# Kernel optimization log

Hardware: AMD Instinct MI355X
Metric: run time of the kernel (lower is better)

## Reference

```python
import jax, jax.numpy as jnp
import numpy as np

RADIUS = 2
ITERATION = 8
KSIZE = 2 * RADIUS + 1


def _side_window_kernels():
    """Build the 8 directional box kernels exactly as in the torch module.
    Returns (8, 1, k, k) float32: order L, R, U, D, NW, NE, SW, SE."""
    r, k = RADIUS, KSIZE
    ones = np.ones((k, k), np.float32)
    L = ones.copy(); L[:, r + 1:] = 0
    R = ones.copy(); R[:, :r] = 0
    U = ones.copy(); U[r + 1:, :] = 0
    D = ones.copy(); D[:r, :] = 0
    # diagonal kernels are cloned from U/D BEFORE normalization (as in source)
    NW, NE, SW, SE = U.copy(), U.copy(), D.copy(), D.copy()
    n_half = (r + 1) * k
    L, R, U, D = L / n_half, R / n_half, U / n_half, D / n_half
    NW[:, r + 1:] = 0; NE[:, :r] = 0; SW[:, r + 1:] = 0; SE[:, :r] = 0
    n_quad = float((r + 1) ** 2)
    NW, NE, SW, SE = NW / n_quad, NE / n_quad, SW / n_quad, SE / n_quad
    return np.stack([L, R, U, D, NW, NE, SW, SE])[:, None]  # (8,1,k,k)


def setup_inputs() -> dict:
    key = jax.random.key(0)
    # HWC image with pixel values in [0, 255)
    img = jax.random.uniform(key, (2048, 2048, 3), dtype=jnp.float32) * 255.0
    return {"img": img}


def reference(img) -> jnp.ndarray:
    kern = jnp.asarray(_side_window_kernels())          # (8,1,k,k)
    x0 = jnp.transpose(img, (2, 0, 1))[:, None]          # (C,1,H,W): channels as batch

    def step(im, _):
        # replicate padding, then valid conv with all 8 directional kernels at once
        p = jnp.pad(im, ((0, 0), (0, 0), (RADIUS, RADIUS), (RADIUS, RADIUS)), mode="edge")
        conv = jax.lax.conv_general_dilated(p, kern, (1, 1), "VALID")  # (C,8,H,W)
        d = conv - im                                    # broadcast (C,1,H,W)->(C,8,H,W)
        idx = jnp.argmin(jnp.abs(d), axis=1, keepdims=True)
        dm = jnp.take_along_axis(d, idx, axis=1)         # (C,1,H,W)
        return im + dm, None

    res, _ = jax.lax.scan(step, x0, None, length=ITERATION)
    diff = jnp.abs(x0 - res)[:, 0]                       # (C,H,W)
    out = jnp.transpose(diff, (1, 2, 0))                 # (H,W,C)
    return jnp.clip(out, 0.0, 255.0)
```

## Files before the change

kernel.cpp:

```cpp
#include <hip/hip_runtime.h>


static constexpr int H  = 2048;
static constexpr int W  = 2048;
static constexpr int C  = 3;
static constexpr int WC = W * C;

template<bool FINAL>
__global__ __launch_bounds__(256)
void swf_step4(const float* __restrict__ src, float* __restrict__ dst,
               const float* __restrict__ x0) {
  const int col4 = (blockIdx.x * 256 + threadIdx.x) * 4;
  const int h    = blockIdx.y;

  const float w15 = 1.0f / 15.0f;
  const float w9  = 1.0f / 9.0f;

  float acc[4][8];
#pragma unroll
  for (int k = 0; k < 4; ++k)
#pragma unroll
    for (int m = 0; m < 8; ++m) acc[k][m] = 0.0f;
  float center[4];

  const bool fastc = (col4 >= 8) && (col4 <= WC - 12);
  if (fastc) {
#pragma unroll
    for (int i = 0; i < 5; ++i) {
      int hy = h + i - 2;
      hy = hy < 0 ? 0 : (hy > H - 1 ? H - 1 : hy);
      const float4* rp = (const float4*)(src + (size_t)hy * WC + (col4 - 8));
      const float4 q0 = rp[0], q1 = rp[1], q2 = rp[2], q3 = rp[3], q4 = rp[4];
      const float r[20] = {q0.x,q0.y,q0.z,q0.w, q1.x,q1.y,q1.z,q1.w,
                           q2.x,q2.y,q2.z,q2.w, q3.x,q3.y,q3.z,q3.w,
                           q4.x,q4.y,q4.z,q4.w};
#pragma unroll
      for (int k = 0; k < 4; ++k) {
        const float t0 = r[k+2], t1 = r[k+5], t2 = r[k+8],
                    t3 = r[k+11], t4 = r[k+14];
        float* a = acc[k];
        if (i == 2) center[k] = t2;
        a[0]=__builtin_fmaf(w15,t0,a[0]); a[0]=__builtin_fmaf(w15,t1,a[0]); a[0]=__builtin_fmaf(w15,t2,a[0]);
        a[1]=__builtin_fmaf(w15,t2,a[1]); a[1]=__builtin_fmaf(w15,t3,a[1]); a[1]=__builtin_fmaf(w15,t4,a[1]);
        if (i <= 2) {
          a[2]=__builtin_fmaf(w15,t0,a[2]); a[2]=__builtin_fmaf(w15,t1,a[2]); a[2]=__builtin_fmaf(w15,t2,a[2]);
          a[2]=__builtin_fmaf(w15,t3,a[2]); a[2]=__builtin_fmaf(w15,t4,a[2]);
          a[4]=__builtin_fmaf(w9,t0,a[4]); a[4]=__builtin_fmaf(w9,t1,a[4]); a[4]=__builtin_fmaf(w9,t2,a[4]);
          a[5]=__builtin_fmaf(w9,t2,a[5]); a[5]=__builtin_fmaf(w9,t3,a[5]); a[5]=__builtin_fmaf(w9,t4,a[5]);
        }
        if (i >= 2) {
          a[3]=__builtin_fmaf(w15,t0,a[3]); a[3]=__builtin_fmaf(w15,t1,a[3]); a[3]=__builtin_fmaf(w15,t2,a[3]);
          a[3]=__builtin_fmaf(w15,t3,a[3]); a[3]=__builtin_fmaf(w15,t4,a[3]);
          a[6]=__builtin_fmaf(w9,t0,a[6]); a[6]=__builtin_fmaf(w9,t1,a[6]); a[6]=__builtin_fmaf(w9,t2,a[6]);
          a[7]=__builtin_fmaf(w9,t2,a[7]); a[7]=__builtin_fmaf(w9,t3,a[7]); a[7]=__builtin_fmaf(w9,t4,a[7]);
        }
      }
    }
  } else {
#pragma unroll
    for (int k = 0; k < 4; ++k) {
      const int col = col4 + k;
      const int w   = col / 3;
      const int c   = col - w * 3;
      int cj[5];
#pragma unroll
      for (int j = 0; j < 5; ++j) {
        int wj = w + j - 2;
        wj = wj < 0 ? 0 : (wj > W - 1 ? W - 1 : wj);
        cj[j] = wj * 3 + c;
      }
      float* a = acc[k];
#pragma unroll
      for (int i = 0; i < 5; ++i) {
        int hy = h + i - 2;
        hy = hy < 0 ? 0 : (hy > H - 1 ? H - 1 : hy);
        const float* r = src + (size_t)hy * WC;
        const float t0 = r[cj[0]], t1 = r[cj[1]], t2 = r[cj[2]],
                    t3 = r[cj[3]], t4 = r[cj[4]];
        if (i == 2) center[k] = t2;
        a[0]=__builtin_fmaf(w15,t0,a[0]); a[0]=__builtin_fmaf(w15,t1,a[0]); a[0]=__builtin_fmaf(w15,t2,a[0]);
        a[1]=__builtin_fmaf(w15,t2,a[1]); a[1]=__builtin_fmaf(w15,t3,a[1]); a[1]=__builtin_fmaf(w15,t4,a[1]);
        if (i <= 2) {
          a[2]=__builtin_fmaf(w15,t0,a[2]); a[2]=__builtin_fmaf(w15,t1,a[2]); a[2]=__builtin_fmaf(w15,t2,a[2]);
          a[2]=__builtin_fmaf(w15,t3,a[2]); a[2]=__builtin_fmaf(w15,t4,a[2]);
          a[4]=__builtin_fmaf(w9,t0,a[4]); a[4]=__builtin_fmaf(w9,t1,a[4]); a[4]=__builtin_fmaf(w9,t2,a[4]);
          a[5]=__builtin_fmaf(w9,t2,a[5]); a[5]=__builtin_fmaf(w9,t3,a[5]); a[5]=__builtin_fmaf(w9,t4,a[5]);
        }
        if (i >= 2) {
          a[3]=__builtin_fmaf(w15,t0,a[3]); a[3]=__builtin_fmaf(w15,t1,a[3]); a[3]=__builtin_fmaf(w15,t2,a[3]);
          a[3]=__builtin_fmaf(w15,t3,a[3]); a[3]=__builtin_fmaf(w15,t4,a[3]);
          a[6]=__builtin_fmaf(w9,t0,a[6]); a[6]=__builtin_fmaf(w9,t1,a[6]); a[6]=__builtin_fmaf(w9,t2,a[6]);
          a[7]=__builtin_fmaf(w9,t2,a[7]); a[7]=__builtin_fmaf(w9,t3,a[7]); a[7]=__builtin_fmaf(w9,t4,a[7]);
        }
      }
    }
  }

  float o[4];
#pragma unroll
  for (int k = 0; k < 4; ++k) {
    float best  = acc[k][0] - center[k];
    float besta = fabsf(best);
#pragma unroll
    for (int m = 1; m < 8; ++m) {
      const float d = acc[k][m] - center[k];
      const float a = fabsf(d);
      if (a < besta) { besta = a; best = d; }
    }
    const float res = center[k] + best;
    if (FINAL) {
      const float xv = x0[(size_t)h * WC + col4 + k];
      float diff = fabsf(xv - res);
      o[k] = diff > 255.0f ? 255.0f : diff;
    } else {
      o[k] = res;
    }
  }
  float4 ov;
  ov.x = o[0]; ov.y = o[1]; ov.z = o[2]; ov.w = o[3];
  *(float4*)(dst + (size_t)h * WC + col4) = ov;
}

extern "C" void kernel_launch(void* const* d_in, const int* in_sizes, int n_in,
                              void* d_out, int out_size, void* d_ws, size_t ws_size,
                              hipStream_t stream) {
  const float* x0  = (const float*)d_in[0];
  float*       out = (float*)d_out;
  float*       ws  = (float*)d_ws;

  dim3 grid(WC / 1024, H);
  dim3 block(256);

  swf_step4<false><<<grid, block, 0, stream>>>(x0,  ws,  nullptr);
  swf_step4<false><<<grid, block, 0, stream>>>(ws,  out, nullptr);
  swf_step4<false><<<grid, block, 0, stream>>>(out, ws,  nullptr);
  swf_step4<false><<<grid, block, 0, stream>>>(ws,  out, nullptr);
  swf_step4<false><<<grid, block, 0, stream>>>(out, ws,  nullptr);
  swf_step4<false><<<grid, block, 0, stream>>>(ws,  out, nullptr);
  swf_step4<false><<<grid, block, 0, stream>>>(out, ws,  nullptr);
  swf_step4<true ><<<grid, block, 0, stream>>>(ws,  out, x0);
}
```

Measured before the change: 463.6 us.

## Process eight rows per thread with rolling register window of input rows

Each thread now computes eight consecutive output rows, keeping a rolling 5-row window of float4 loads in registers so each input row is loaded once per thread instead of five times. The grid shrinks in the row dimension by the same factor. This cuts redundant global/L2 load traffic and instruction issue for loads, at the cost of higher register pressure (25 float4 plus accumulators) and fewer blocks for latency hiding.

New measurement: 509.2 us. 1.1x slower.

```diff
diff --git a/kernel.cpp b/kernel.cpp
--- a/kernel.cpp
+++ b/kernel.cpp
@@ -1,124 +1,186 @@
 #include <hip/hip_runtime.h>
 
 
-static constexpr int H  = 2048;
-static constexpr int W  = 2048;
-static constexpr int C  = 3;
-static constexpr int WC = W * C;
+static constexpr int H   = 2048;
+static constexpr int W   = 2048;
+static constexpr int C   = 3;
+static constexpr int WC  = W * C;
+static constexpr int RPT = 8;
 
 template<bool FINAL>
 __global__ __launch_bounds__(256)
-void swf_step4(const float* __restrict__ src, float* __restrict__ dst,
-               const float* __restrict__ x0) {
+void swf_roll(const float* __restrict__ src, float* __restrict__ dst,
+              const float* __restrict__ x0) {
   const int col4 = (blockIdx.x * 256 + threadIdx.x) * 4;
-  const int h    = blockIdx.y;
+  const int h0   = blockIdx.y * RPT;
 
   const float w15 = 1.0f / 15.0f;
   const float w9  = 1.0f / 9.0f;
 
-  float acc[4][8];
-#pragma unroll
-  for (int k = 0; k < 4; ++k)
-#pragma unroll
-    for (int m = 0; m < 8; ++m) acc[k][m] = 0.0f;
-  float center[4];
-
   const bool fastc = (col4 >= 8) && (col4 <= WC - 12);
   if (fastc) {
-#pragma unroll
-    for (int i = 0; i < 5; ++i) {
-      int hy = h + i - 2;
-      hy = hy < 0 ? 0 : (hy > H - 1 ? H - 1 : hy);
-      const float4* rp = (const float4*)(src + (size_t)hy * WC + (col4 - 8));
-      const float4 q0 = rp[0], q1 = rp[1], q2 = rp[2], q3 = rp[3], q4 = rp[4];
-      const float r[20] = {q0.x,q0.y,q0.z,q0.w, q1.x,q1.y,q1.z,q1.w,
-                           q2.x,q2.y,q2.z,q2.w, q3.x,q3.y,q3.z,q3.w,
-                           q4.x,q4.y,q4.z,q4.w};
+    const float* colbase = src + (col4 - 8);
+    float4 q[5][5];
+
+#pragma unroll
+    for (int p = 0; p < 4; ++p) {
+      int hy = h0 + p - 2;
+      hy = hy < 0 ? 0 : hy;
+      const float4* rp = (const float4*)(colbase + (size_t)hy * WC);
+#pragma unroll
+      for (int j = 0; j < 5; ++j) q[p][j] = rp[j];
+    }
+
+#pragma unroll
+    for (int t = 0; t < RPT; ++t) {
+      {
+        int hy = h0 + t + 2;
+        hy = hy > H - 1 ? H - 1 : hy;
+        const float4* rp = (const float4*)(colbase + (size_t)hy * WC);
+#pragma unroll
+        for (int j = 0; j < 5; ++j) q[(t + 4) % 5][j] = rp[j];
+      }
+
+      float acc[4][8];
+#pragma unroll
+      for (int k = 0; k < 4; ++k)
+#pragma unroll
+        for (int m = 0; m < 8; ++m) acc[k][m] = 0.0f;
+      float center[4];
+
+#pragma unroll
+      for (int i = 0; i < 5; ++i) {
+        const int s = (t + i) % 5;
+        const float r[20] = {q[s][0].x,q[s][0].y,q[s][0].z,q[s][0].w,
+                             q[s][1].x,q[s][1].y,q[s][1].z,q[s][1].w,
+                             q[s][2].x,q[s][2].y,q[s][2].z,q[s][2].w,
+                             q[s][3].x,q[s][3].y,q[s][3].z,q[s][3].w,
+                             q[s][4].x,q[s][4].y,q[s][4].z,q[s][4].w};
+#pragma unroll
+        for (int k = 0; k < 4; ++k) {
+          const float t0 = r[k+2], t1 = r[k+5], t2 = r[k+8],
+                      t3 = r[k+11], t4 = r[k+14];
+          float* a = acc[k];
+          if (i == 2) center[k] = t2;
+          a[0]=__builtin_fmaf(w15,t0,a[0]); a[0]=__builtin_fmaf(w15,t1,a[0]); a[0]=__builtin_fmaf(w15,t2,a[0]);
+          a[1]=__builtin_fmaf(w15,t2,a[1]); a[1]=__builtin_fmaf(w15,t3,a[1]); a[1]=__builtin_fmaf(w15,t4,a[1]);
+          if (i <= 2) {
+            a[2]=__builtin_fmaf(w15,t0,a[2]); a[2]=__builtin_fmaf(w15,t1,a[2]); a[2]=__builtin_fmaf(w15,t2,a[2]);
+            a[2]=__builtin_fmaf(w15,t3,a[2]); a[2]=__builtin_fmaf(w15,t4,a[2]);
+            a[4]=__builtin_fmaf(w9,t0,a[4]); a[4]=__builtin_fmaf(w9,t1,a[4]); a[4]=__builtin_fmaf(w9,t2,a[4]);
+            a[5]=__builtin_fmaf(w9,t2,a[5]); a[5]=__builtin_fmaf(w9,t3,a[5]); a[5]=__builtin_fmaf(w9,t4,a[5]);
+          }
+          if (i >= 2) {
+            a[3]=__builtin_fmaf(w15,t0,a[3]); a[3]=__builtin_fmaf(w15,t1,a[3]); a[3]=__builtin_fmaf(w15,t2,a[3]);
+            a[3]=__builtin_fmaf(w15,t3,a[3]); a[3]=__builtin_fmaf(w15,t4,a[3]);
+            a[6]=__builtin_fmaf(w9,t0,a[6]); a[6]=__builtin_fmaf(w9,t1,a[6]); a[6]=__builtin_fmaf(w9,t2,a[6]);
+            a[7]=__builtin_fmaf(w9,t2,a[7]); a[7]=__builtin_fmaf(w9,t3,a[7]); a[7]=__builtin_fmaf(w9,t4,a[7]);
+          }
+        }
+      }
+
+      const int y = h0 + t;
+      float4 xv4;
+      if (FINAL) xv4 = *(const float4*)(x0 + (size_t)y * WC + col4);
+      float o[4];
 #pragma unroll
       for (int k = 0; k < 4; ++k) {
-        const float t0 = r[k+2], t1 = r[k+5], t2 = r[k+8],
-                    t3 = r[k+11], t4 = r[k+14];
-        float* a = acc[k];
-        if (i == 2) center[k] = t2;
-        a[0]=__builtin_fmaf(w15,t0,a[0]); a[0]=__builtin_fmaf(w15,t1,a[0]); a[0]=__builtin_fmaf(w15,t2,a[0]);
-        a[1]=__builtin_fmaf(w15,t2,a[1]); a[1]=__builtin_fmaf(w15,t3,a[1]); a[1]=__builtin_fmaf(w15,t4,a[1]);
-        if (i <= 2) {
-          a[2]=__builtin_fmaf(w15,t0,a[2]); a[2]=__builtin_fmaf(w15,t1,a[2]); a[2]=__builtin_fmaf(w15,t2,a[2]);
-          a[2]=__builtin_fmaf(w15,t3,a[2]); a[2]=__builtin_fmaf(w15,t4,a[2]);
-          a[4]=__builtin_fmaf(w9,t0,a[4]); a[4]=__builtin_fmaf(w9,t1,a[4]); a[4]=__builtin_fmaf(w9,t2,a[4]);
-          a[5]=__builtin_fmaf(w9,t2,a[5]); a[5]=__builtin_fmaf(w9,t3,a[5]); a[5]=__builtin_fmaf(w9,t4,a[5]);
-        }
-        if (i >= 2) {
-          a[3]=__builtin_fmaf(w15,t0,a[3]); a[3]=__builtin_fmaf(w15,t1,a[3]); a[3]=__builtin_fmaf(w15,t2,a[3]);
-          a[3]=__builtin_fmaf(w15,t3,a[3]); a[3]=__builtin_fmaf(w15,t4,a[3]);
-          a[6]=__builtin_fmaf(w9,t0,a[6]); a[6]=__builtin_fmaf(w9,t1,a[6]); a[6]=__builtin_fmaf(w9,t2,a[6]);
-          a[7]=__builtin_fmaf(w9,t2,a[7]); a[7]=__builtin_fmaf(w9,t3,a[7]); a[7]=__builtin_fmaf(w9,t4,a[7]);
-        }
-      }
+        float best  = acc[k][0] - center[k];
+        float besta = fabsf(best);
+#pragma unroll
+        for (int m = 1; m < 8; ++m) {
+          const float d = acc[k][m] - center[k];
+          const float a = fabsf(d);
+          if (a < besta) { besta = a; best = d; }
+        }
+        const float res = center[k] + best;
+        if (FINAL) {
+          const float xv = (k == 0) ? xv4.x : (k == 1) ? xv4.y
+                         : (k == 2) ? xv4.z : xv4.w;
+          float diff = fabsf(xv - res);
+          o[k] = diff > 255.0f ? 255.0f : diff;
+        } else {
+          o[k] = res;
+        }
+      }
+      float4 ov;
+      ov.x = o[0]; ov.y = o[1]; ov.z = o[2]; ov.w = o[3];
+      *(float4*)(dst + (size_t)y * WC + col4) = ov;
     }
   } else {
+    int cjk[4][5];
 #pragma unroll
     for (int k = 0; k < 4; ++k) {
       const int col = col4 + k;
       const int w   = col / 3;
       const int c   = col - w * 3;
-      int cj[5];
 #pragma unroll
       for (int j = 0; j < 5; ++j) {
         int wj = w + j - 2;
         wj = wj < 0 ? 0 : (wj > W - 1 ? W - 1 : wj);
-        cj[j] = wj * 3 + c;
-      }
-      float* a = acc[k];
-#pragma unroll
-      for (int i = 0; i < 5; ++i) {
-        int hy = h + i - 2;
-        hy = hy < 0 ? 0 : (hy > H - 1 ? H - 1 : hy);
-        const float* r = src + (size_t)hy * WC;
-        const float t0 = r[cj[0]], t1 = r[cj[1]], t2 = r[cj[2]],
-                    t3 = r[cj[3]], t4 = r[cj[4]];
-        if (i == 2) center[k] = t2;
-        a[0]=__builtin_fmaf(w15,t0,a[0]); a[0]=__builtin_fmaf(w15,t1,a[0]); a[0]=__builtin_fmaf(w15,t2,a[0]);
-        a[1]=__builtin_fmaf(w15,t2,a[1]); a[1]=__builtin_fmaf(w15,t3,a[1]); a[1]=__builtin_fmaf(w15,t4,a[1]);
-        if (i <= 2) {
-          a[2]=__builtin_fmaf(w15,t0,a[2]); a[2]=__builtin_fmaf(w15,t1,a[2]); a[2]=__builtin_fmaf(w15,t2,a[2]);
-          a[2]=__builtin_fmaf(w15,t3,a[2]); a[2]=__builtin_fmaf(w15,t4,a[2]);
-          a[4]=__builtin_fmaf(w9,t0,a[4]); a[4]=__builtin_fmaf(w9,t1,a[4]); a[4]=__builtin_fmaf(w9,t2,a[4]);
-          a[5]=__builtin_fmaf(w9,t2,a[5]); a[5]=__builtin_fmaf(w9,t3,a[5]); a[5]=__builtin_fmaf(w9,t4,a[5]);
-        }
-        if (i >= 2) {
-          a[3]=__builtin_fmaf(w15,t0,a[3]); a[3]=__builtin_fmaf(w15,t1,a[3]); a[3]=__builtin_fmaf(w15,t2,a[3]);
-          a[3]=__builtin_fmaf(w15,t3,a[3]); a[3]=__builtin_fmaf(w15,t4,a[3]);
-          a[6]=__builtin_fmaf(w9,t0,a[6]); a[6]=__builtin_fmaf(w9,t1,a[6]); a[6]=__builtin_fmaf(w9,t2,a[6]);
-          a[7]=__builtin_fmaf(w9,t2,a[7]); a[7]=__builtin_fmaf(w9,t3,a[7]); a[7]=__builtin_fmaf(w9,t4,a[7]);
-        }
-      }
+        cjk[k][j] = wj * 3 + c;
+      }
+    }
+    for (int t = 0; t < RPT; ++t) {
+      const int y = h0 + t;
+      float acc[4][8];
+#pragma unroll
+      for (int k = 0; k < 4; ++k)
+#pragma unroll
+        for (int m = 0; m < 8; ++m) acc[k][m] = 0.0f;
+      float center[4];
+#pragma unroll
+      for (int k = 0; k < 4; ++k) {
+        float* a = acc[k];
+#pragma unroll
+        for (int i = 0; i < 5; ++i) {
+          int hy = y + i - 2;
+          hy = hy < 0 ? 0 : (hy > H - 1 ? H - 1 : hy);
+          const float* r = src + (size_t)hy * WC;
+          const float t0 = r[cjk[k][0]], t1 = r[cjk[k][1]], t2 = r[cjk[k][2]],
+                      t3 = r[cjk[k][3]], t4 = r[cjk[k][4]];
+          if (i == 2) center[k] = t2;
+          a[0]=__builtin_fmaf(w15,t0,a[0]); a[0]=__builtin_fmaf(w15,t1,a[0]); a[0]=__builtin_fmaf(w15,t2,a[0]);
+          a[1]=__builtin_fmaf(w15,t2,a[1]); a[1]=__builtin_fmaf(w15,t3,a[1]); a[1]=__builtin_fmaf(w15,t4,a[1]);
+          if (i <= 2) {
+            a[2]=__builtin_fmaf(w15,t0,a[2]); a[2]=__builtin_fmaf(w15,t1,a[2]); a[2]=__builtin_fmaf(w15,t2,a[2]);
+            a[2]=__builtin_fmaf(w15,t3,a[2]); a[2]=__builtin_fmaf(w15,t4,a[2]);
+            a[4]=__builtin_fmaf(w9,t0,a[4]); a[4]=__builtin_fmaf(w9,t1,a[4]); a[4]=__builtin_fmaf(w9,t2,a[4]);
+            a[5]=__builtin_fmaf(w9,t2,a[5]); a[5]=__builtin_fmaf(w9,t3,a[5]); a[5]=__builtin_fmaf(w9,t4,a[5]);
+          }
+          if (i >= 2) {
+            a[3]=__builtin_fmaf(w15,t0,a[3]); a[3]=__builtin_fmaf(w15,t1,a[3]); a[3]=__builtin_fmaf(w15,t2,a[3]);
+            a[3]=__builtin_fmaf(w15,t3,a[3]); a[3]=__builtin_fmaf(w15,t4,a[3]);
+            a[6]=__builtin_fmaf(w9,t0,a[6]); a[6]=__builtin_fmaf(w9,t1,a[6]); a[6]=__builtin_fmaf(w9,t2,a[6]);
+            a[7]=__builtin_fmaf(w9,t2,a[7]); a[7]=__builtin_fmaf(w9,t3,a[7]); a[7]=__builtin_fmaf(w9,t4,a[7]);
+          }
+        }
+      }
+      float o[4];
+#pragma unroll
+      for (int k = 0; k < 4; ++k) {
+        float best  = acc[k][0] - center[k];
+        float besta = fabsf(best);
+#pragma unroll
+        for (int m = 1; m < 8; ++m) {
+          const float d = acc[k][m] - center[k];
+          const float a = fabsf(d);
+          if (a < besta) { besta = a; best = d; }
+        }
+        const float res = center[k] + best;
+        if (FINAL) {
+          const float xv = x0[(size_t)y * WC + col4 + k];
+          float diff = fabsf(xv - res);
+          o[k] = diff > 255.0f ? 255.0f : diff;
+        } else {
+          o[k] = res;
+        }
+      }
+      float4 ov;
+      ov.x = o[0]; ov.y = o[1]; ov.z = o[2]; ov.w = o[3];
+      *(float4*)(dst + (size_t)y * WC + col4) = ov;
     }
   }
-
-  float o[4];
-#pragma unroll
-  for (int k = 0; k < 4; ++k) {
-    float best  = acc[k][0] - center[k];
-    float besta = fabsf(best);
-#pragma unroll
-    for (int m = 1; m < 8; ++m) {
-      const float d = acc[k][m] - center[k];
-      const float a = fabsf(d);
-      if (a < besta) { besta = a; best = d; }
-    }
-    const float res = center[k] + best;
-    if (FINAL) {
-      const float xv = x0[(size_t)h * WC + col4 + k];
-      float diff = fabsf(xv - res);
-      o[k] = diff > 255.0f ? 255.0f : diff;
-    } else {
-      o[k] = res;
-    }
-  }
-  float4 ov;
-  ov.x = o[0]; ov.y = o[1]; ov.z = o[2]; ov.w = o[3];
-  *(float4*)(dst + (size_t)h * WC + col4) = ov;
 }
 
 extern "C" void kernel_launch(void* const* d_in, const int* in_sizes, int n_in,
@@ -128,15 +190,15 @@
   float*       out = (float*)d_out;
   float*       ws  = (float*)d_ws;
 
-  dim3 grid(WC / 1024, H);
+  dim3 grid(WC / 1024, H / RPT);
   dim3 block(256);
 
-  swf_step4<false><<<grid, block, 0, stream>>>(x0,  ws,  nullptr);
-  swf_step4<false><<<grid, block, 0, stream>>>(ws,  out, nullptr);
-  swf_step4<false><<<grid, block, 0, stream>>>(out, ws,  nullptr);
-  swf_step4<false><<<grid, block, 0, stream>>>(ws,  out, nullptr);
-  swf_step4<false><<<grid, block, 0, stream>>>(out, ws,  nullptr);
-  swf_step4<false><<<grid, block, 0, stream>>>(ws,  out, nullptr);
-  swf_step4<false><<<grid, block, 0, stream>>>(out, ws,  nullptr);
-  swf_step4<true ><<<grid, block, 0, stream>>>(ws,  out, x0);
+  swf_roll<false><<<grid, block, 0, stream>>>(x0,  ws,  nullptr);
+  swf_roll<false><<<grid, block, 0, stream>>>(ws,  out, nullptr);
+  swf_roll<false><<<grid, block, 0, stream>>>(out, ws,  nullptr);
+  swf_roll<false><<<grid, block, 0, stream>>>(ws,  out, nullptr);
+  swf_roll<false><<<grid, block, 0, stream>>>(out, ws,  nullptr);
+  swf_roll<false><<<grid, block, 0, stream>>>(ws,  out, nullptr);
+  swf_roll<false><<<grid, block, 0, stream>>>(out, ws,  nullptr);
+  swf_roll<true ><<<grid, block, 0, stream>>>(ws,  out, x0);
 }
```

## Stage halo tiles in LDS and compute eight rows per block

Applied to the files above, without the earlier changes.

Replaces the per-row global-memory stencil with a tiled kernel. Each 128-thread block loads a 12-row by 532-float halo tile into shared memory, with edge replication handled during the load, then loops over 8 output rows reading the 5x5 window from LDS. This removes the repeated global and L2 reads of overlapping rows and the slow scalar boundary path. In exchange it adds a __syncthreads, a serial row loop that limits parallelism per block, and LDS read traffic that may cause bank conflicts.

Measured after the change: 530.2 us. 14.4% more time.

```diff
diff --git a/kernel.cpp b/kernel.cpp
--- a/kernel.cpp
+++ b/kernel.cpp
@@ -1,36 +1,76 @@
 #include <hip/hip_runtime.h>
 
 
-static constexpr int H  = 2048;
-static constexpr int W  = 2048;
-static constexpr int C  = 3;
-static constexpr int WC = W * C;
+static constexpr int H     = 2048;
+static constexpr int W     = 2048;
+static constexpr int C     = 3;
+static constexpr int WC    = W * C;
+static constexpr int RPT   = 8;
+static constexpr int TPB   = 128;
+static constexpr int BCOLS = TPB * 4;
+static constexpr int RW    = BCOLS + 20;
+static constexpr int NROWS = RPT + 4;
+static constexpr int NCH   = RW / 4;
 
 template<bool FINAL>
-__global__ __launch_bounds__(256)
-void swf_step4(const float* __restrict__ src, float* __restrict__ dst,
-               const float* __restrict__ x0) {
-  const int col4 = (blockIdx.x * 256 + threadIdx.x) * 4;
-  const int h    = blockIdx.y;
+__global__ __launch_bounds__(TPB)
+void swf_lds(const float* __restrict__ src, float* __restrict__ dst,
+             const float* __restrict__ x0) {
+  __shared__ __align__(16) float s[NROWS][RW];
+
+  const int tid  = threadIdx.x;
+  const int bx   = blockIdx.x;
+  const int y0   = blockIdx.y * RPT;
+  const int base = bx * BCOLS - 8;
+
+  for (int r = 0; r < NROWS; ++r) {
+    int hy = y0 + r - 2;
+    hy = hy < 0 ? 0 : (hy > H - 1 ? H - 1 : hy);
+    const float* srow = src + (size_t)hy * WC;
+    for (int cc = tid; cc < NCH; cc += TPB) {
+      const int gp = base + cc * 4;
+      float4 v;
+      if (gp >= 0 && gp + 3 < WC) {
+        v = *(const float4*)(srow + gp);
+      } else {
+        float tmp[4];
+#pragma unroll
+        for (int u = 0; u < 4; ++u) {
+          const int f = gp + u;
+          const int idx = (f < 0)    ? ((f % 3) + 3) % 3
+                        : (f >= WC)  ? (W - 1) * 3 + (f % 3)
+                        : f;
+          tmp[u] = srow[idx];
+        }
+        v.x = tmp[0]; v.y = tmp[1]; v.z = tmp[2]; v.w = tmp[3];
+      }
+      *(float4*)&s[r][cc * 4] = v;
+    }
+  }
+  __syncthreads();
 
   const float w15 = 1.0f / 15.0f;
   const float w9  = 1.0f / 9.0f;
+  const int   lc   = tid * 4;
+  const int   col4 = bx * BCOLS + tid * 4;
 
-  float acc[4][8];
+#pragma unroll 1
+  for (int t = 0; t < RPT; ++t) {
+    float acc[4][8];
 #pragma unroll
-  for (int k = 0; k < 4; ++k)
+    for (int k = 0; k < 4; ++k)
 #pragma unroll
-    for (int m = 0; m < 8; ++m) acc[k][m] = 0.0f;
-  float center[4];
+      for (int m = 0; m < 8; ++m) acc[k][m] = 0.0f;
+    float center[4];
 
-  const bool fastc = (col4 >= 8) && (col4 <= WC - 12);
-  if (fastc) {
 #pragma unroll
     for (int i = 0; i < 5; ++i) {
-      int hy = h + i - 2;
-      hy = hy < 0 ? 0 : (hy > H - 1 ? H - 1 : hy);
-      const float4* rp = (const float4*)(src + (size_t)hy * WC + (col4 - 8));
-      const float4 q0 = rp[0], q1 = rp[1], q2 = rp[2], q3 = rp[3], q4 = rp[4];
+      const float* row = &s[t + i][lc];
+      const float4 q0 = *(const float4*)(row);
+      const float4 q1 = *(const float4*)(row + 4);
+      const float4 q2 = *(const float4*)(row + 8);
+      const float4 q3 = *(const float4*)(row + 12);
+      const float4 q4 = *(const float4*)(row + 16);
       const float r[20] = {q0.x,q0.y,q0.z,q0.w, q1.x,q1.y,q1.z,q1.w,
                            q2.x,q2.y,q2.z,q2.w, q3.x,q3.y,q3.z,q3.w,
                            q4.x,q4.y,q4.z,q4.w};
@@ -56,69 +96,35 @@
         }
       }
     }
-  } else {
+
+    const int y = y0 + t;
+    float4 xv4;
+    if (FINAL) xv4 = *(const float4*)(x0 + (size_t)y * WC + col4);
+    float o[4];
 #pragma unroll
     for (int k = 0; k < 4; ++k) {
-      const int col = col4 + k;
-      const int w   = col / 3;
-      const int c   = col - w * 3;
-      int cj[5];
+      float best  = acc[k][0] - center[k];
+      float besta = fabsf(best);
 #pragma unroll
-      for (int j = 0; j < 5; ++j) {
-        int wj = w + j - 2;
-        wj = wj < 0 ? 0 : (wj > W - 1 ? W - 1 : wj);
-        cj[j] = wj * 3 + c;
+      for (int m = 1; m < 8; ++m) {
+        const float d = acc[k][m] - center[k];
+        const float a = fabsf(d);
+        if (a < besta) { besta = a; best = d; }
       }
-      float* a = acc[k];
-#pragma unroll
-      for (int i = 0; i < 5; ++i) {
-        int hy = h + i - 2;
-        hy = hy < 0 ? 0 : (hy > H - 1 ? H - 1 : hy);
-        const float* r = src + (size_t)hy * WC;
-        const float t0 = r[cj[0]], t1 = r[cj[1]], t2 = r[cj[2]],
-                    t3 = r[cj[3]], t4 = r[cj[4]];
-        if (i == 2) center[k] = t2;
-        a[0]=__builtin_fmaf(w15,t0,a[0]); a[0]=__builtin_fmaf(w15,t1,a[0]); a[0]=__builtin_fmaf(w15,t2,a[0]);
-        a[1]=__builtin_fmaf(w15,t2,a[1]); a[1]=__builtin_fmaf(w15,t3,a[1]); a[1]=__builtin_fmaf(w15,t4,a[1]);
-        if (i <= 2) {
-          a[2]=__builtin_fmaf(w15,t0,a[2]); a[2]=__builtin_fmaf(w15,t1,a[2]); a[2]=__builtin_fmaf(w15,t2,a[2]);
-          a[2]=__builtin_fmaf(w15,t3,a[2]); a[2]=__builtin_fmaf(w15,t4,a[2]);
-          a[4]=__builtin_fmaf(w9,t0,a[4]); a[4]=__builtin_fmaf(w9,t1,a[4]); a[4]=__builtin_fmaf(w9,t2,a[4]);
-          a[5]=__builtin_fmaf(w9,t2,a[5]); a[5]=__builtin_fmaf(w9,t3,a[5]); a[5]=__builtin_fmaf(w9,t4,a[5]);
-        }
-        if (i >= 2) {
-          a[3]=__builtin_fmaf(w15,t0,a[3]); a[3]=__builtin_fmaf(w15,t1,a[3]); a[3]=__builtin_fmaf(w15,t2,a[3]);
-          a[3]=__builtin_fmaf(w15,t3,a[3]); a[3]=__builtin_fmaf(w15,t4,a[3]);
-          a[6]=__builtin_fmaf(w9,t0,a[6]); a[6]=__builtin_fmaf(w9,t1,a[6]); a[6]=__builtin_fmaf(w9,t2,a[6]);
-          a[7]=__builtin_fmaf(w9,t2,a[7]); a[7]=__builtin_fmaf(w9,t3,a[7]); a[7]=__builtin_fmaf(w9,t4,a[7]);
-        }
+      const float res = center[k] + best;
+      if (FINAL) {
+        const float xv = (k == 0) ? xv4.x : (k == 1) ? xv4.y
+                       : (k == 2) ? xv4.z : xv4.w;
+        float diff = fabsf(xv - res);
+        o[k] = diff > 255.0f ? 255.0f : diff;
+      } else {
+        o[k] = res;
       }
     }
+    float4 ov;
+    ov.x = o[0]; ov.y = o[1]; ov.z = o[2]; ov.w = o[3];
+    *(float4*)(dst + (size_t)y * WC + col4) = ov;
   }
-
-  float o[4];
-#pragma unroll
-  for (int k = 0; k < 4; ++k) {
-    float best  = acc[k][0] - center[k];
-    float besta = fabsf(best);
-#pragma unroll
-    for (int m = 1; m < 8; ++m) {
-      const float d = acc[k][m] - center[k];
-      const float a = fabsf(d);
-      if (a < besta) { besta = a; best = d; }
-    }
-    const float res = center[k] + best;
-    if (FINAL) {
-      const float xv = x0[(size_t)h * WC + col4 + k];
-      float diff = fabsf(xv - res);
-      o[k] = diff > 255.0f ? 255.0f : diff;
-    } else {
-      o[k] = res;
-    }
-  }
-  float4 ov;
-  ov.x = o[0]; ov.y = o[1]; ov.z = o[2]; ov.w = o[3];
-  *(float4*)(dst + (size_t)h * WC + col4) = ov;
 }
 
 extern "C" void kernel_launch(void* const* d_in, const int* in_sizes, int n_in,
@@ -128,15 +134,15 @@
   float*       out = (float*)d_out;
   float*       ws  = (float*)d_ws;
 
-  dim3 grid(WC / 1024, H);
-  dim3 block(256);
+  dim3 grid(WC / BCOLS, H / RPT);
+  dim3 block(TPB);
 
-  swf_step4<false><<<grid, block, 0, stream>>>(x0,  ws,  nullptr);
-  swf_step4<false><<<grid, block, 0, stream>>>(ws,  out, nullptr);
-  swf_step4<false><<<grid, block, 0, stream>>>(out, ws,  nullptr);
-  swf_step4<false><<<grid, block, 0, stream>>>(ws,  out, nullptr);
-  swf_step4<false><<<grid, block, 0, stream>>>(out, ws,  nullptr);
-  swf_step4<false><<<grid, block, 0, stream>>>(ws,  out, nullptr);
-  swf_step4<false><<<grid, block, 0, stream>>>(out, ws,  nullptr);
-  swf_step4<true ><<<grid, block, 0, stream>>>(ws,  out, x0);
+  swf_lds<false><<<grid, block, 0, stream>>>(x0,  ws,  nullptr);
+  swf_lds<false><<<grid, block, 0, stream>>>(ws,  out, nullptr);
+  swf_lds<false><<<grid, block, 0, stream>>>(out, ws,  nullptr);
+  swf_lds<false><<<grid, block, 0, stream>>>(ws,  out, nullptr);
+  swf_lds<false><<<grid, block, 0, stream>>>(out, ws,  nullptr);
+  swf_lds<false><<<grid, block, 0, stream>>>(ws,  out, nullptr);
+  swf_lds<false><<<grid, block, 0, stream>>>(out, ws,  nullptr);
+  swf_lds<true ><<<grid, block, 0, stream>>>(ws,  out, x0);
 }
```
